# Optimization experiments

Measured on AMD Instinct MI355X. Metric: run time of the kernel, lower is better.

## Reference

```python
import jax, jax.numpy as jnp
import numpy as np

B, T, D, H = 16, 1024, 2048, 512


def _lstm_dir(x, w_ih, w_hh, b_ih, b_hh, reverse):
    # x: (B,T,Din); w_ih: (4H,Din); w_hh: (4H,H). PyTorch gate order: i,f,g,o.
    h_dim = w_hh.shape[1]
    xg = jnp.einsum('btd,gd->btg', x, w_ih) + b_ih + b_hh  # (B,T,4H) input gates precomputed

    def step(carry, xg_t):
        h, c = carry
        g = xg_t + h @ w_hh.T
        i, f, gg, o = jnp.split(g, 4, axis=-1)
        i = jax.nn.sigmoid(i)
        f = jax.nn.sigmoid(f)
        gg = jnp.tanh(gg)
        o = jax.nn.sigmoid(o)
        c = f * c + i * gg
        h = o * jnp.tanh(c)
        return (h, c), h

    b = x.shape[0]
    init = (jnp.zeros((b, h_dim), x.dtype), jnp.zeros((b, h_dim), x.dtype))
    _, hs = jax.lax.scan(step, init, jnp.swapaxes(xg, 0, 1), reverse=reverse)
    return jnp.swapaxes(hs, 0, 1)  # (B,T,H)


def _bilstm_layer(x, p_fwd, p_bwd):
    out_f = _lstm_dir(x, *p_fwd, reverse=False)
    out_b = _lstm_dir(x, *p_bwd, reverse=True)
    return jnp.concatenate([out_f, out_b], axis=-1)  # (B,T,2H)


def setup_inputs() -> dict:
    key = jax.random.key(0)
    ks = jax.random.split(key, 20)
    s = 1.0 / np.sqrt(H)

    def u(k, shape):
        return jax.random.uniform(k, shape, jnp.float32, -s, s)

    inp = {'x': jax.random.normal(ks[0], (B, T, D), jnp.float32)}
    i = 1
    for layer, din in [(0, D), (1, 2 * H)]:
        for suf in ['', '_rev']:
            inp[f'w_ih_l{layer}{suf}'] = u(ks[i], (4 * H, din)); i += 1
            inp[f'w_hh_l{layer}{suf}'] = u(ks[i], (4 * H, H)); i += 1
            inp[f'b_ih_l{layer}{suf}'] = u(ks[i], (4 * H,)); i += 1
            inp[f'b_hh_l{layer}{suf}'] = u(ks[i], (4 * H,)); i += 1
            i -= 2  # reuse keys sparingly
            inp[f'b_ih_l{layer}{suf}'] = u(jax.random.fold_in(ks[i], 1), (4 * H,))
            inp[f'b_hh_l{layer}{suf}'] = u(jax.random.fold_in(ks[i], 2), (4 * H,))
            i += 2
    inp['attn_w'] = u(ks[17], (1, 2 * H))
    inp['attn_b'] = u(ks[18], (1,))
    return inp


def reference(x,
              w_ih_l0, w_hh_l0, b_ih_l0, b_hh_l0,
              w_ih_l0_rev, w_hh_l0_rev, b_ih_l0_rev, b_hh_l0_rev,
              w_ih_l1, w_hh_l1, b_ih_l1, b_hh_l1,
              w_ih_l1_rev, w_hh_l1_rev, b_ih_l1_rev, b_hh_l1_rev,
              attn_w, attn_b):
    out = _bilstm_layer(x,
                        (w_ih_l0, w_hh_l0, b_ih_l0, b_hh_l0),
                        (w_ih_l0_rev, w_hh_l0_rev, b_ih_l0_rev, b_hh_l0_rev))
    out = _bilstm_layer(out,
                        (w_ih_l1, w_hh_l1, b_ih_l1, b_hh_l1),
                        (w_ih_l1_rev, w_hh_l1_rev, b_ih_l1_rev, b_hh_l1_rev))
    # attention pooling: Linear(2H -> 1), softmax over time, weighted sum
    scores = jnp.einsum('bth,oh->bto', out, attn_w) + attn_b  # (B,T,1)
    weights = jax.nn.softmax(scores, axis=1)
    encoding = jnp.sum(weights * out, axis=1)  # (B, 2H)
    return encoding
```

## Files before the change

kernel.cpp:

```cpp
#include <hip/hip_runtime.h>
#include <hip/hip_bf16.h>
#include <cstdio>

typedef unsigned short ushort_t;
typedef unsigned long long u64;
typedef __attribute__((ext_vector_type(4))) float f32x4;
typedef __attribute__((ext_vector_type(4))) unsigned int u32x4;
typedef __attribute__((ext_vector_type(8))) __bf16 bf16x8;
typedef __attribute__((ext_vector_type(8))) unsigned short u16x8;
typedef __attribute__((ext_vector_type(4))) unsigned short u16x4;

#define B_  16
#define T_  1024
#define H_  512
#define NG  2048
#define M_  (B_*T_)
#define NBLK_DIR 16
#define FLG_DIR  256

__device__ inline unsigned short f2bf_rne(float f){
  union { float f; unsigned int u; } v; v.f = f;
  unsigned int u = v.u;
  unsigned int r = (u + 0x7fffu + ((u >> 16) & 1u)) >> 16;
  return (unsigned short)r;
}
__device__ inline float bf2f(unsigned short s){
  union { unsigned int u; float f; } v; v.u = ((unsigned int)s) << 16;
  return v.f;
}
__device__ inline float sigm_f(float x){
  return 1.0f / (1.0f + __expf(-x));
}
__device__ inline float tanh_f(float x){
  return 1.0f - 2.0f / (__expf(2.0f * x) + 1.0f);
}

__global__ void zero_u32(unsigned* __restrict__ p, int n){
  int i = blockIdx.x * blockDim.x + threadIdx.x;
  if (i < n) p[i] = 0u;
}

__device__ inline void split_range(const float* __restrict__ src,
                                   ushort_t* __restrict__ hi, ushort_t* __restrict__ lo,
                                   int n4, int idx, int stride){
  for (int i = idx; i < n4; i += stride){
    f32x4 v = ((const f32x4*)src)[i];
    u16x4 h4, l4;
    #pragma unroll
    for (int j = 0; j < 4; j++){
      unsigned short h = f2bf_rne(v[j]);
      h4[j] = h;
      l4[j] = f2bf_rne(v[j] - bf2f(h));
    }
    ((u16x4*)hi)[i] = h4;
    ((u16x4*)lo)[i] = l4;
  }
}

__global__ void split_f32_bf16(const float* __restrict__ src,
                               ushort_t* __restrict__ hi, ushort_t* __restrict__ lo,
                               int n4){
  split_range(src, hi, lo, n4,
              blockIdx.x * blockDim.x + threadIdx.x, gridDim.x * blockDim.x);
}

__global__ __launch_bounds__(256) void gemm_xg(
    const ushort_t* __restrict__ Ahi, const ushort_t* __restrict__ Alo,
    const ushort_t* __restrict__ Bhi0, const ushort_t* __restrict__ Blo0,
    const ushort_t* __restrict__ Bhi1, const ushort_t* __restrict__ Blo1,
    const float* __restrict__ bi0, const float* __restrict__ bh0,
    const float* __restrict__ bi1, const float* __restrict__ bh1,
    float* __restrict__ C0, float* __restrict__ C1,
    int M, int N, int K)
{
  __shared__ ushort_t As[128*32];
  __shared__ ushort_t Bs[128*32];
  const int tid  = threadIdx.x;
  const int wave = tid >> 6, lane = tid & 63;
  const int l15 = lane & 15, l4 = lane >> 4;
  const int wr = wave >> 1, wc = wave & 1;
  const int n0 = blockIdx.x * 128, m0 = blockIdx.y * 128;
  const int dir = blockIdx.z;
  const ushort_t* Bhi = dir ? Bhi1 : Bhi0;
  const ushort_t* Blo = dir ? Blo1 : Blo0;
  const float* bia = dir ? bi1 : bi0;
  const float* bib = dir ? bh1 : bh0;
  float* C = dir ? C1 : C0;

  f32x4 acc[4][4];
  #pragma unroll
  for (int i = 0; i < 4; i++)
    #pragma unroll
    for (int j = 0; j < 4; j++) acc[i][j] = (f32x4){0.f,0.f,0.f,0.f};

  const int e0 = tid, e1 = 256 + tid;
  const int row0 = e0 >> 2, c80 = (e0 & 3) * 8;
  const int row1 = e1 >> 2, c81 = (e1 & 3) * 8;

  for (int seg = 0; seg < 3; ++seg){
    const ushort_t* Ap = (seg == 2) ? Alo : Ahi;
    const ushort_t* Bp = (seg == 1) ? Blo : Bhi;
    for (int kt = 0; kt < K; kt += 32){
      __builtin_amdgcn_global_load_lds(
        (const __attribute__((address_space(1))) unsigned int*)(Ap + (size_t)(m0 + row0) * K + kt + c80),
        (__attribute__((address_space(3))) unsigned int*)(As + e0 * 8), 16, 0, 0);
      __builtin_amdgcn_global_load_lds(
        (const __attribute__((address_space(1))) unsigned int*)(Bp + (size_t)(n0 + row0) * K + kt + c80),
        (__attribute__((address_space(3))) unsigned int*)(Bs + e0 * 8), 16, 0, 0);
      __builtin_amdgcn_global_load_lds(
        (const __attribute__((address_space(1))) unsigned int*)(Ap + (size_t)(m0 + row1) * K + kt + c81),
        (__attribute__((address_space(3))) unsigned int*)(As + e1 * 8), 16, 0, 0);
      __builtin_amdgcn_global_load_lds(
        (const __attribute__((address_space(1))) unsigned int*)(Bp + (size_t)(n0 + row1) * K + kt + c81),
        (__attribute__((address_space(3))) unsigned int*)(Bs + e1 * 8), 16, 0, 0);
      __syncthreads();
      bf16x8 af[4], bfr[4];
      #pragma unroll
      for (int m = 0; m < 4; m++)
        af[m] = *(const bf16x8*)(As + (wr*64 + m*16 + l15) * 32 + l4 * 8);
      #pragma unroll
      for (int n = 0; n < 4; n++)
        bfr[n] = *(const bf16x8*)(Bs + (wc*64 + n*16 + l15) * 32 + l4 * 8);
      #pragma unroll
      for (int m = 0; m < 4; m++)
        #pragma unroll
        for (int n = 0; n < 4; n++)
          acc[m][n] = __builtin_amdgcn_mfma_f32_16x16x32_bf16(af[m], bfr[n], acc[m][n], 0, 0, 0);
      __syncthreads();
    }
  }
  #pragma unroll
  for (int m = 0; m < 4; m++)
    #pragma unroll
    for (int n = 0; n < 4; n++){
      int col = n0 + wc*64 + n*16 + l15;
      float bias = bia[col] + bib[col];
      #pragma unroll
      for (int r = 0; r < 4; r++){
        int row = m0 + wr*64 + m*16 + l4*4 + r;
        C[(size_t)row * N + col] = acc[m][n][r] + bias;
      }
    }
}

__global__ __launch_bounds__(512, 1) void lstm_layer(
    const float* __restrict__ whh_fwd, const float* __restrict__ whh_bwd,
    const float* __restrict__ xg,
    unsigned* __restrict__ hbuf,
    unsigned* __restrict__ flags,
    float* __restrict__ out_f32,
    ushort_t* __restrict__ out_hi,
    ushort_t* __restrict__ out_lo,
    const float* __restrict__ spl_src0, ushort_t* __restrict__ spl_hi0,
    ushort_t* __restrict__ spl_lo0, int spl_n0,
    const float* __restrict__ spl_src1, ushort_t* __restrict__ spl_hi1,
    ushort_t* __restrict__ spl_lo1, int spl_n1)
{
  const int tid = threadIdx.x;

  if (blockIdx.x >= 2 * NBLK_DIR){
    const int idx = (blockIdx.x - 2 * NBLK_DIR) * 512 + tid;
    const int stride = (gridDim.x - 2 * NBLK_DIR) * 512;
    if (spl_src0) split_range(spl_src0, spl_hi0, spl_lo0, spl_n0, idx, stride);
    if (spl_src1) split_range(spl_src1, spl_hi1, spl_lo1, spl_n1, idx, stride);
    return;
  }

  const int dir = blockIdx.x >> 4;
  const int cb  = blockIdx.x & 15;
  const int wave = tid >> 6, lane = tid & 63;
  const int gate = wave >> 1, ch = wave & 1;
  const int l15 = lane & 15, l4 = lane >> 4;
  const float* whh = dir ? whh_bwd : whh_fwd;
  unsigned* hb = hbuf + (size_t)dir * 2 * 8192;
  unsigned* flg = flags + (size_t)dir * FLG_DIR;

  __shared__ ushort_t hfhi[8192];
  __shared__ ushort_t hflo[8192];
  __shared__ float gbuf[4][16][33];
  __shared__ unsigned s_token;

  bf16x8 Whi[16], Wlo[16];
  {
    const int wrow = gate * 512 + cb * 32 + ch * 16 + l15;
    const float* p0 = whh + (size_t)wrow * 512;
    #pragma unroll
    for (int s = 0; s < 16; s++){
      const float* p = p0 + s * 32 + l4 * 8;
      f32x4 va = *(const f32x4*)(p);
      f32x4 vb = *(const f32x4*)(p + 4);
      u16x8 th, tl;
      #pragma unroll
      for (int j = 0; j < 4; j++){
        unsigned short h = f2bf_rne(va[j]);
        th[j] = h; tl[j] = f2bf_rne(va[j] - bf2f(h));
        unsigned short h2 = f2bf_rne(vb[j]);
        th[4+j] = h2; tl[4+j] = f2bf_rne(vb[j] - bf2f(h2));
      }
      Whi[s] = __builtin_bit_cast(bf16x8, th);
      Wlo[s] = __builtin_bit_cast(bf16x8, tl);
    }
  }

  const int eb = tid >> 5, ecl = tid & 31, ecol = cb * 32 + ecl;

  const int p   = tid >> 5;
  const int b5  = tid & 31;
  const int cb_b  = b5 >> 1;
  const int lo1 = b5 & 1;
  const int unitBase = (p * 4 + lo1 * 2) * 16 + cb_b;

  if (tid == 0) s_token = 0u;
  __hip_atomic_store(&hb[cb * 512 + tid], 0u, __ATOMIC_RELAXED, __HIP_MEMORY_SCOPE_AGENT);
  __syncthreads();
  if (tid < NBLK_DIR)
    __hip_atomic_store(&flg[tid * NBLK_DIR + cb], 1u, __ATOMIC_RELAXED, __HIP_MEMORY_SCOPE_AGENT);

  float c_state = 0.0f;

  for (int t = 0; t < T_; ++t){
    const int t_eff = dir ? (T_ - 1 - t) : t;
    const float* xgp = xg + ((size_t)dir * M_ + (size_t)eb * T_ + t_eff) * NG + ecol;
    float xi = xgp[0];
    float xf = xgp[512];
    float xgg = xgp[1024];
    float xo = xgp[1536];

    const unsigned want = (unsigned)(t + 1);
    if (wave == 0){
      if (lane < NBLK_DIR){
        const unsigned* f = &flg[cb * NBLK_DIR + lane];
        while (__hip_atomic_load(f, __ATOMIC_RELAXED, __HIP_MEMORY_SCOPE_AGENT) < want)
          __builtin_amdgcn_s_sleep(1);
      }
      if (lane == 0)
        __hip_atomic_store(&s_token, want, __ATOMIC_RELEASE, __HIP_MEMORY_SCOPE_WORKGROUP);
    } else {
      while (__hip_atomic_load(&s_token, __ATOMIC_ACQUIRE, __HIP_MEMORY_SCOPE_WORKGROUP) < want)
        __builtin_amdgcn_s_sleep(1);
    }

    const u64* src = (const u64*)(hb + (size_t)(t & 1) * 8192) + (size_t)p * 256 + (size_t)b5 * 8;
    u64 v[8];
    #pragma unroll
    for (int k = 0; k < 8; k++)
      v[k] = __hip_atomic_load(&src[k], __ATOMIC_RELAXED, __HIP_MEMORY_SCOPE_AGENT);

    {
      u32x4 wh0, wh1, wl0, wl1;
      #pragma unroll
      for (int k = 0; k < 4; k++){
        unsigned d0 = (unsigned)v[k], d1 = (unsigned)(v[k] >> 32);
        wh0[k] = (d0 & 0xffffu) | (d1 << 16);
        wl0[k] = (d0 >> 16) | (d1 & 0xffff0000u);
      }
      #pragma unroll
      for (int k = 0; k < 4; k++){
        unsigned d0 = (unsigned)v[4 + k], d1 = (unsigned)(v[4 + k] >> 32);
        wh1[k] = (d0 & 0xffffu) | (d1 << 16);
        wl1[k] = (d0 >> 16) | (d1 & 0xffff0000u);
      }
      ((u32x4*)hfhi)[unitBase]      = wh0;
      ((u32x4*)hfhi)[unitBase + 16] = wh1;
      ((u32x4*)hflo)[unitBase]      = wl0;
      ((u32x4*)hflo)[unitBase + 16] = wl1;
    }
    __syncthreads();

    {
      f32x4 a0 = {0.f,0.f,0.f,0.f}, a1 = a0, a2 = a0;
      #pragma unroll
      for (int s = 0; s < 16; s++){
        bf16x8 ah = *(const bf16x8*)&hfhi[(s * 64 + l4 * 16 + l15) * 8];
        bf16x8 al = *(const bf16x8*)&hflo[(s * 64 + l4 * 16 + l15) * 8];
        a0 = __builtin_amdgcn_mfma_f32_16x16x32_bf16(ah, Whi[s], a0, 0, 0, 0);
        a1 = __builtin_amdgcn_mfma_f32_16x16x32_bf16(ah, Wlo[s], a1, 0, 0, 0);
        a2 = __builtin_amdgcn_mfma_f32_16x16x32_bf16(al, Whi[s], a2, 0, 0, 0);
      }
      f32x4 acc = a0 + a1;
      acc = acc + a2;
      #pragma unroll
      for (int r = 0; r < 4; r++)
        gbuf[gate][l4 * 4 + r][ch * 16 + l15] = acc[r];
    }
    __syncthreads();

    float h; unsigned short hh, hl; size_t oidx;
    {
      float pi = gbuf[0][eb][ecl] + xi;
      float pf = gbuf[1][eb][ecl] + xf;
      float pg = gbuf[2][eb][ecl] + xgg;
      float po = gbuf[3][eb][ecl] + xo;
      float ig = sigm_f(pi);
      float fg = sigm_f(pf);
      float gg = tanh_f(pg);
      float og = sigm_f(po);
      c_state = fg * c_state + ig * gg;
      h = og * tanh_f(c_state);
      hh = f2bf_rne(h);
      hl = f2bf_rne(h - bf2f(hh));
      oidx = ((size_t)eb * T_ + t_eff) * 1024 + dir * 512 + ecol;
      __hip_atomic_store(&hb[(size_t)((t + 1) & 1) * 8192 + cb * 512 + tid],
                         (unsigned)hh | ((unsigned)hl << 16),
                         __ATOMIC_RELAXED, __HIP_MEMORY_SCOPE_AGENT);
    }
    __syncthreads();
    if (tid < NBLK_DIR)
      __hip_atomic_store(&flg[tid * NBLK_DIR + cb], (unsigned)(t + 2),
                         __ATOMIC_RELAXED, __HIP_MEMORY_SCOPE_AGENT);
    if (out_f32) out_f32[oidx] = h;
    if (out_hi){ out_hi[oidx] = hh; out_lo[oidx] = hl; }
  }
}

__device__ inline float dot4(f32x4 a, f32x4 b){
  return a[0]*b[0] + a[1]*b[1] + a[2]*b[2] + a[3]*b[3];
}

__global__ __launch_bounds__(256) void attn_pool(
    const float* __restrict__ out1,
    const float* __restrict__ aw,
    const float* __restrict__ ab,
    float* __restrict__ enc)
{
  __shared__ float wbuf[1024];
  __shared__ float sc[1024];
  __shared__ float red[16];
  const int b = blockIdx.x;
  const int tid = threadIdx.x;
  const int wave = tid >> 6, lane = tid & 63;
  ((f32x4*)wbuf)[tid] = ((const f32x4*)aw)[tid];
  __syncthreads();
  const float* ob = out1 + (size_t)b * T_ * 1024;
  const float bias = ab[0];

  for (int t = wave; t < T_; t += 4){
    const float* row = ob + (size_t)t * 1024;
    float s = dot4(((const f32x4*)row)[lane],       ((const f32x4*)wbuf)[lane])
            + dot4(((const f32x4*)row)[lane + 64],  ((const f32x4*)wbuf)[lane + 64])
            + dot4(((const f32x4*)row)[lane + 128], ((const f32x4*)wbuf)[lane + 128])
            + dot4(((const f32x4*)row)[lane + 192], ((const f32x4*)wbuf)[lane + 192]);
    #pragma unroll
    for (int o = 32; o > 0; o >>= 1) s += __shfl_xor(s, o, 64);
    if (lane == 0) sc[t] = s + bias;
  }
  __syncthreads();

  float m = -1e30f;
  for (int i = tid; i < 1024; i += 256) m = fmaxf(m, sc[i]);
  #pragma unroll
  for (int o = 32; o > 0; o >>= 1) m = fmaxf(m, __shfl_xor(m, o, 64));
  if (lane == 0) red[wave] = m;
  __syncthreads();
  m = fmaxf(fmaxf(red[0], red[1]), fmaxf(red[2], red[3]));

  float ssum = 0.f;
  for (int i = tid; i < 1024; i += 256){
    float p = __expf(sc[i] - m);
    sc[i] = p;
    ssum += p;
  }
  #pragma unroll
  for (int o = 32; o > 0; o >>= 1) ssum += __shfl_xor(ssum, o, 64);
  if (lane == 0) red[8 + wave] = ssum;
  __syncthreads();
  float inv = 1.0f / (red[8] + red[9] + red[10] + red[11]);

  f32x4 a = {0.f,0.f,0.f,0.f};
  for (int t = 0; t < T_; t++){
    f32x4 v = *(const f32x4*)(ob + (size_t)t * 1024 + tid * 4);
    float p = sc[t];
    a[0] += p * v[0]; a[1] += p * v[1]; a[2] += p * v[2]; a[3] += p * v[3];
  }
  f32x4 r = { a[0]*inv, a[1]*inv, a[2]*inv, a[3]*inv };
  *(f32x4*)(enc + (size_t)b * 1024 + tid * 4) = r;
}

extern "C" void kernel_launch(void* const* d_in, const int* in_sizes, int n_in,
                              void* d_out, int out_size, void* d_ws, size_t ws_size,
                              hipStream_t stream)
{
  const float* x        = (const float*)d_in[0];
  const float* w_ih_l0  = (const float*)d_in[1];
  const float* w_hh_l0  = (const float*)d_in[2];
  const float* b_ih_l0  = (const float*)d_in[3];
  const float* b_hh_l0  = (const float*)d_in[4];
  const float* w_ih_l0r = (const float*)d_in[5];
  const float* w_hh_l0r = (const float*)d_in[6];
  const float* b_ih_l0r = (const float*)d_in[7];
  const float* b_hh_l0r = (const float*)d_in[8];
  const float* w_ih_l1  = (const float*)d_in[9];
  const float* w_hh_l1  = (const float*)d_in[10];
  const float* b_ih_l1  = (const float*)d_in[11];
  const float* b_hh_l1  = (const float*)d_in[12];
  const float* w_ih_l1r = (const float*)d_in[13];
  const float* w_hh_l1r = (const float*)d_in[14];
  const float* b_ih_l1r = (const float*)d_in[15];
  const float* b_hh_l1r = (const float*)d_in[16];
  const float* attn_w   = (const float*)d_in[17];
  const float* attn_b   = (const float*)d_in[18];
  float* enc = (float*)d_out;

  char* ws = (char*)d_ws;
  size_t off = 0;
  auto alloc = [&](size_t bytes) -> void* {
    void* p = ws + off;
    off += (bytes + 255) & ~(size_t)255;
    return p;
  };
  ushort_t* Ahi  = (ushort_t*)alloc((size_t)M_ * 2048 * 2);
  ushort_t* Alo  = (ushort_t*)alloc((size_t)M_ * 2048 * 2);
  ushort_t* Whi0 = (ushort_t*)alloc((size_t)2048 * 2048 * 2);
  ushort_t* Wlo0 = (ushort_t*)alloc((size_t)2048 * 2048 * 2);
  ushort_t* Whi1 = (ushort_t*)alloc((size_t)2048 * 2048 * 2);
  ushort_t* Wlo1 = (ushort_t*)alloc((size_t)2048 * 2048 * 2);
  float*    xg   = (float*)alloc((size_t)2 * M_ * NG * 4);
  float*    outb = (float*)alloc((size_t)M_ * 1024 * 4);
  unsigned* hbuf = (unsigned*)alloc((size_t)2 * 2 * 2 * 8192 * 4);
  unsigned* flags= (unsigned*)alloc((size_t)2 * 2 * FLG_DIR * 4);
  if (off > ws_size){
    fprintf(stderr, "kernel_launch: workspace too small: need %zu have %zu\n", off, ws_size);
    return;
  }

  {
    int n = 2 * 2 * 2 * 8192 + 2 * 2 * FLG_DIR;
    zero_u32<<<(n + 255) / 256, 256, 0, stream>>>(hbuf, n);
  }

  split_f32_bf16<<<2048, 256, 0, stream>>>(x, Ahi, Alo, M_ * 2048 / 4);
  split_f32_bf16<<<512, 256, 0, stream>>>(w_ih_l0,  Whi0, Wlo0, 2048 * 2048 / 4);
  split_f32_bf16<<<512, 256, 0, stream>>>(w_ih_l0r, Whi1, Wlo1, 2048 * 2048 / 4);
  gemm_xg<<<dim3(16, 128, 2), 256, 0, stream>>>(
      Ahi, Alo, Whi0, Wlo0, Whi1, Wlo1,
      b_ih_l0, b_hh_l0, b_ih_l0r, b_hh_l0r,
      xg, xg + (size_t)M_ * NG, M_, NG, 2048);
  lstm_layer<<<256, 512, 0, stream>>>(w_hh_l0, w_hh_l0r, xg, hbuf, flags,
                                      nullptr, Ahi, Alo,
                                      w_ih_l1,  Whi0, Wlo0, 2048 * 1024 / 4,
                                      w_ih_l1r, Whi1, Wlo1, 2048 * 1024 / 4);
  gemm_xg<<<dim3(16, 128, 2), 256, 0, stream>>>(
      Ahi, Alo, Whi0, Wlo0, Whi1, Wlo1,
      b_ih_l1, b_hh_l1, b_ih_l1r, b_hh_l1r,
      xg, xg + (size_t)M_ * NG, M_, NG, 1024);
  lstm_layer<<<32, 512, 0, stream>>>(w_hh_l1, w_hh_l1r, xg,
                                     hbuf + (size_t)2 * 2 * 8192,
                                     flags + (size_t)2 * FLG_DIR,
                                     outb, nullptr, nullptr,
                                     nullptr, nullptr, nullptr, 0,
                                     nullptr, nullptr, nullptr, 0);
  attn_pool<<<16, 256, 0, stream>>>(outb, attn_w, attn_b, enc);
}
```

Before: 10.07 ms.

## Replace per-block flag barrier with per-wave fine-grained flags in LSTM recurrence

Each wave now publishes its own progress flag for every consumer block after a vmcnt wait, and each consumer thread polls only the single flag covering the h slice it reads. This removes the wave-0 poll plus LDS token handoff and the second __syncthreads per timestep. The goal is to shorten the critical-path cross-block handshake in the sequential recurrence. In exchange the flag array grows and there are more atomic stores per step, and correctness depends on the flag-to-slice mapping and on the vmcnt wait ordering the h store before the flag store.

After: 10.88 ms. 8.1% more time.

```diff
diff --git a/kernel.cpp b/kernel.cpp
--- a/kernel.cpp
+++ b/kernel.cpp
@@ -16,7 +16,7 @@
 #define NG  2048
 #define M_  (B_*T_)
 #define NBLK_DIR 16
-#define FLG_DIR  256
+#define FLG_DIR  2048
 
 __device__ inline unsigned short f2bf_rne(float f){
   union { float f; unsigned int u; } v; v.f = f;
@@ -178,7 +178,6 @@
   __shared__ ushort_t hfhi[8192];
   __shared__ ushort_t hflo[8192];
   __shared__ float gbuf[4][16][33];
-  __shared__ unsigned s_token;
 
   bf16x8 Whi[16], Wlo[16];
   {
@@ -209,12 +208,12 @@
   const int cb_b  = b5 >> 1;
   const int lo1 = b5 & 1;
   const int unitBase = (p * 4 + lo1 * 2) * 16 + cb_b;
-
-  if (tid == 0) s_token = 0u;
+  const unsigned* my_flag = &flg[cb * 128 + p * 8 + (b5 >> 2)];
+
   __hip_atomic_store(&hb[cb * 512 + tid], 0u, __ATOMIC_RELAXED, __HIP_MEMORY_SCOPE_AGENT);
-  __syncthreads();
-  if (tid < NBLK_DIR)
-    __hip_atomic_store(&flg[tid * NBLK_DIR + cb], 1u, __ATOMIC_RELAXED, __HIP_MEMORY_SCOPE_AGENT);
+  asm volatile("s_waitcnt vmcnt(0)" ::: "memory");
+  if (lane < NBLK_DIR)
+    __hip_atomic_store(&flg[lane * 128 + cb * 8 + wave], 1u, __ATOMIC_RELAXED, __HIP_MEMORY_SCOPE_AGENT);
 
   float c_state = 0.0f;
 
@@ -227,18 +226,8 @@
     float xo = xgp[1536];
 
     const unsigned want = (unsigned)(t + 1);
-    if (wave == 0){
-      if (lane < NBLK_DIR){
-        const unsigned* f = &flg[cb * NBLK_DIR + lane];
-        while (__hip_atomic_load(f, __ATOMIC_RELAXED, __HIP_MEMORY_SCOPE_AGENT) < want)
-          __builtin_amdgcn_s_sleep(1);
-      }
-      if (lane == 0)
-        __hip_atomic_store(&s_token, want, __ATOMIC_RELEASE, __HIP_MEMORY_SCOPE_WORKGROUP);
-    } else {
-      while (__hip_atomic_load(&s_token, __ATOMIC_ACQUIRE, __HIP_MEMORY_SCOPE_WORKGROUP) < want)
-        __builtin_amdgcn_s_sleep(1);
-    }
+    while (__hip_atomic_load(my_flag, __ATOMIC_RELAXED, __HIP_MEMORY_SCOPE_AGENT) < want)
+      __builtin_amdgcn_s_sleep(1);
 
     const u64* src = (const u64*)(hb + (size_t)(t & 1) * 8192) + (size_t)p * 256 + (size_t)b5 * 8;
     u64 v[8];
@@ -285,7 +274,6 @@
     }
     __syncthreads();
 
-    float h; unsigned short hh, hl; size_t oidx;
     {
       float pi = gbuf[0][eb][ecl] + xi;
       float pf = gbuf[1][eb][ecl] + xf;
@@ -296,20 +284,20 @@
       float gg = tanh_f(pg);
       float og = sigm_f(po);
       c_state = fg * c_state + ig * gg;
-      h = og * tanh_f(c_state);
-      hh = f2bf_rne(h);
-      hl = f2bf_rne(h - bf2f(hh));
-      oidx = ((size_t)eb * T_ + t_eff) * 1024 + dir * 512 + ecol;
+      float h = og * tanh_f(c_state);
+      unsigned short hh = f2bf_rne(h);
+      unsigned short hl = f2bf_rne(h - bf2f(hh));
       __hip_atomic_store(&hb[(size_t)((t + 1) & 1) * 8192 + cb * 512 + tid],
                          (unsigned)hh | ((unsigned)hl << 16),
                          __ATOMIC_RELAXED, __HIP_MEMORY_SCOPE_AGENT);
-    }
-    __syncthreads();
-    if (tid < NBLK_DIR)
-      __hip_atomic_store(&flg[tid * NBLK_DIR + cb], (unsigned)(t + 2),
-                         __ATOMIC_RELAXED, __HIP_MEMORY_SCOPE_AGENT);
-    if (out_f32) out_f32[oidx] = h;
-    if (out_hi){ out_hi[oidx] = hh; out_lo[oidx] = hl; }
+      asm volatile("s_waitcnt vmcnt(0)" ::: "memory");
+      if (lane < NBLK_DIR)
+        __hip_atomic_store(&flg[lane * 128 + cb * 8 + wave], (unsigned)(t + 2),
+                           __ATOMIC_RELAXED, __HIP_MEMORY_SCOPE_AGENT);
+      size_t oidx = ((size_t)eb * T_ + t_eff) * 1024 + dir * 512 + ecol;
+      if (out_f32) out_f32[oidx] = h;
+      if (out_hi){ out_hi[oidx] = hh; out_lo[oidx] = hl; }
+    }
   }
 }
 
```
